# Optimization experiments

Hardware: AMD Instinct MI355X
Metric: run time of the kernel (lower is better)

## Reference

```python
import jax, jax.numpy as jnp
import numpy as np
from math import sqrt

THRESHOLD = 0.5
NEG_POS_RATIO = 3
ALPHA = 1.0


def make_priors():
    fms = [(38, 0.1, [1.0, 2.0, 0.5]), (19, 0.2, [1.0, 2.0, 0.5, 3.0, 1.0 / 3]),
           (10, 0.375, [1.0, 2.0, 0.5, 3.0, 1.0 / 3]), (5, 0.55, [1.0, 2.0, 0.5, 3.0, 1.0 / 3]),
           (3, 0.725, [1.0, 2.0, 0.5]), (1, 0.9, [1.0, 2.0, 0.5])]
    scales = [0.1, 0.2, 0.375, 0.55, 0.725, 0.9]
    priors = []
    for k, (d, s, ratios) in enumerate(fms):
        for i in range(d):
            for j in range(d):
                cx = (i + 0.5) / d
                cy = (j + 0.5) / d
                for r in ratios:
                    priors.append([cx, cy, s * sqrt(r), s / sqrt(r)])
                    if r == 1.0:
                        add = sqrt(scales[k] * scales[k + 1]) if k + 1 < len(scales) else 1.0
                        priors.append([cx, cy, add, add])
    return np.clip(np.asarray(priors, dtype=np.float32), 0.0, 1.0)  # [8732, 4]


def cxcy_to_xy(b):
    return jnp.concatenate([b[..., :2] - b[..., 2:] / 2.0, b[..., :2] + b[..., 2:] / 2.0], -1)


def jaccard(a, b):
    # a: [O,4] cxcy, b: [P,4] cxcy -> IoU [O,P]
    a_xy, b_xy = cxcy_to_xy(a), cxcy_to_xy(b)
    lt = jnp.maximum(a_xy[:, None, :2], b_xy[None, :, :2])
    rb = jnp.minimum(a_xy[:, None, 2:], b_xy[None, :, 2:])
    wh = jnp.clip(rb - lt, 0.0)
    inter = wh[..., 0] * wh[..., 1]
    area_a = (a_xy[:, 2] - a_xy[:, 0]) * (a_xy[:, 3] - a_xy[:, 1])
    area_b = (b_xy[:, 2] - b_xy[:, 0]) * (b_xy[:, 3] - b_xy[:, 1])
    return inter / (area_a[:, None] + area_b[None, :] - inter)


def cxcy_to_gcxgcy(cxcy, priors):
    g_cxcy = (cxcy[..., :2] - priors[..., :2]) / (priors[..., 2:] / 10.0)
    g_wh = jnp.log(cxcy[..., 2:] / priors[..., 2:]) * 5.0
    return jnp.concatenate([g_cxcy, g_wh], -1)


def match_one(boxes_i, priors):
    # boxes_i: [O,4] cxcy
    n_obj = boxes_i.shape[0]
    ov = jaccard(boxes_i, priors)                      # [O, P]
    ov_per_prior = ov.max(0)                           # [P]
    obj_per_prior = ov.argmax(0)                       # [P]
    prior_per_obj = ov.argmax(1)                       # [O]
    obj_per_prior = obj_per_prior.at[prior_per_obj].set(jnp.arange(n_obj))
    ov_per_prior = ov_per_prior.at[prior_per_obj].set(1.0)
    labels = (ov_per_prior >= THRESHOLD).astype(jnp.int32)  # [P], 1=text 0=bg
    true_locs = cxcy_to_gcxgcy(boxes_i[obj_per_prior], priors)  # [P,4]
    return labels, true_locs


def setup_inputs() -> dict:
    key = jax.random.key(0)
    k1, k2, k3, k4 = jax.random.split(key, 4)
    priors = jnp.asarray(make_priors())
    B, P, O = 512, priors.shape[0], 16
    predicted_locs = jax.random.normal(k1, (B, P, 4), dtype=jnp.float32)
    predicted_scores = jax.random.normal(k2, (B, P, 2), dtype=jnp.float32)
    centers = 0.2 + 0.6 * jax.random.uniform(k3, (B, O, 2), dtype=jnp.float32)
    wh = 0.05 + 0.35 * jax.random.uniform(k4, (B, O, 2), dtype=jnp.float32)
    boxes = jnp.concatenate([centers, wh], -1)  # cxcy format
    return {"predicted_locs": predicted_locs, "predicted_scores": predicted_scores,
            "boxes": boxes, "priors": priors}


def reference(predicted_locs, predicted_scores, boxes, priors):
    B, P, _ = predicted_locs.shape
    labels, true_locs = jax.vmap(match_one, in_axes=(0, None))(boxes, priors)  # [B,P], [B,P,4]
    pos = labels != 0
    mask = pos.astype(predicted_locs.dtype)            # [B,P]
    n_pos = pos.sum(1)                                 # [B]

    # localization L1 loss (mean over positive box coordinates)
    loc_abs = jnp.abs(predicted_locs - true_locs).sum(-1)  # [B,P]
    loc_loss = (loc_abs * mask).sum() / (mask.sum() * 4.0)

    # per-prior cross-entropy
    logp = jax.nn.log_softmax(predicted_scores, -1)
    ce = -jnp.take_along_axis(logp, labels[..., None], -1)[..., 0]  # [B,P]

    conf_pos = (ce * mask).sum()
    ce_neg = jnp.where(pos, 0.0, ce)
    ce_neg = jnp.sort(ce_neg, axis=1)[:, ::-1]         # descending
    hard = jnp.arange(P)[None, :] < (NEG_POS_RATIO * n_pos)[:, None]
    conf_hn = (ce_neg * hard.astype(ce_neg.dtype)).sum()
    conf_loss = (conf_pos + conf_hn) / n_pos.sum().astype(predicted_locs.dtype)
    return conf_loss + ALPHA * loc_loss
```

## Files before the change

kernel.cpp:

```cpp
#include <hip/hip_runtime.h>

#define NP 8732
#define NQ (NP / 4)
#define NPT 35
#define NO 16
#define BLK 256
#define NWAVE (BLK / 64)
#define SPLIT 4
#define CHUNK (NP / SPLIT)


__global__ __launch_bounds__(BLK, 8) void match_kernel(
    const float* __restrict__ boxes,
    const float* __restrict__ priors,
    unsigned char* __restrict__ g_obj,
    float* __restrict__ g_bv,
    int*   __restrict__ g_bi)
{
    const int b    = blockIdx.x;
    const int s    = blockIdx.y;
    const int tid  = threadIdx.x;
    const int lane = tid & 63;
    const int wv   = tid >> 6;
    const int quad = tid & 3;
    const int objLo = quad << 2;
    const int lo = s * CHUNK, hi = lo + CHUNK;

    __shared__ float s_bxy[NO][4];
    __shared__ float s_barea[NO];
    __shared__ float s_redv[NO * NWAVE];
    __shared__ int   s_redi[NO * NWAVE];

    if (tid < NO) {
        const float* bx = boxes + (size_t)b * NO * 4 + tid * 4;
        float cx = bx[0], cy = bx[1], w = bx[2], h = bx[3];
        s_bxy[tid][0] = cx - w * 0.5f; s_bxy[tid][1] = cy - h * 0.5f;
        s_bxy[tid][2] = cx + w * 0.5f; s_bxy[tid][3] = cy + h * 0.5f;
        s_barea[tid] = w * h;
    }
    __syncthreads();

    float rx0[4], ry0[4], rx1[4], ry1[4], ra[4];
#pragma unroll
    for (int j = 0; j < 4; j++) {
        rx0[j] = s_bxy[objLo + j][0]; ry0[j] = s_bxy[objLo + j][1];
        rx1[j] = s_bxy[objLo + j][2]; ry1[j] = s_bxy[objLo + j][3];
        ra[j]  = s_barea[objLo + j];
    }

    float tbv[4]; int tbp[4];
#pragma unroll
    for (int j = 0; j < 4; j++) { tbv[j] = -1.0f; tbp[j] = lo; }

    unsigned char* obj_row = g_obj + (size_t)b * NP;
    for (int p = lo + (tid >> 2); p < hi; p += (BLK / 4)) {
        float4 pr = ((const float4*)priors)[p];
        float px0 = pr.x - pr.z * 0.5f, py0 = pr.y - pr.w * 0.5f;
        float px1 = pr.x + pr.z * 0.5f, py1 = pr.y + pr.w * 0.5f;
        float areab = pr.z * pr.w;
        float bv = -1.0f; int bo = objLo;
#pragma unroll
        for (int j = 0; j < 4; j++) {
            float ix0 = fmaxf(rx0[j], px0);
            float iy0 = fmaxf(ry0[j], py0);
            float ix1 = fminf(rx1[j], px1);
            float iy1 = fminf(ry1[j], py1);
            float iw = fmaxf(ix1 - ix0, 0.0f);
            float ih = fmaxf(iy1 - iy0, 0.0f);
            float inter = iw * ih;
            float den = ra[j] + areab - inter;
            float iou = inter * __builtin_amdgcn_rcpf(den);
            if (iou > bv)     { bv = iou; bo = objLo + j; }
            if (iou > tbv[j]) { tbv[j] = iou; tbp[j] = p; }
        }
        float vN = __shfl_xor(bv, 1, 64);
        int   oN = __shfl_xor(bo, 1, 64);
        bool take = (quad & 1) ? (vN >= bv) : (vN > bv);
        if (take) { bv = vN; bo = oN; }
        vN = __shfl_xor(bv, 2, 64);
        oN = __shfl_xor(bo, 2, 64);
        take = (quad & 2) ? (vN >= bv) : (vN > bv);
        if (take) { bv = vN; bo = oN; }
        if (quad == 0) {
            bool pos = (bv >= 0.5f);
            obj_row[p] = (unsigned char)(bo | (pos ? 0x80 : 0));
        }
    }

#pragma unroll
    for (int j = 0; j < 4; j++) {
        float v = tbv[j]; int i = tbp[j];
        for (int off = 32; off >= 4; off >>= 1) {
            float v2 = __shfl_down(v, off, 64);
            int   i2 = __shfl_down(i, off, 64);
            if (v2 > v || (v2 == v && i2 < i)) { v = v2; i = i2; }
        }
        if (lane < 4) {
            s_redv[(objLo + j) * NWAVE + wv] = v;
            s_redi[(objLo + j) * NWAVE + wv] = i;
        }
    }
    __syncthreads();
    if (tid < NO) {
        float v = s_redv[tid * NWAVE]; int i = s_redi[tid * NWAVE];
#pragma unroll
        for (int w = 1; w < NWAVE; w++) {
            float v2 = s_redv[tid * NWAVE + w]; int i2 = s_redi[tid * NWAVE + w];
            if (v2 > v || (v2 == v && i2 < i)) { v = v2; i = i2; }
        }
        g_bv[((size_t)b * NO + tid) * SPLIT + s] = v;
        g_bi[((size_t)b * NO + tid) * SPLIT + s] = i;
    }
}

__device__ __forceinline__ int hist_select(unsigned* hist, unsigned* s_part,
                                           unsigned* s_csuf, unsigned* s_sel,
                                           unsigned& kk, int tid, int lane, int wv)
{
    unsigned ps = 0;
#pragma unroll
    for (int i = 0; i < 16; i++) ps += hist[tid * 16 + i];
    s_part[tid] = ps;
    __syncthreads();
    if (wv == 0) {
        unsigned c0 = s_part[4 * lane + 0], c1 = s_part[4 * lane + 1];
        unsigned c2 = s_part[4 * lane + 2], c3 = s_part[4 * lane + 3];
        unsigned g = c0 + c1 + c2 + c3;
        unsigned incl = g;
#pragma unroll
        for (int off = 1; off < 64; off <<= 1) {
            unsigned o = __shfl_down(incl, off, 64);
            if (lane + off < 64) incl += o;
        }
        unsigned excl = incl - g;
        s_csuf[4 * lane + 3] = excl;
        s_csuf[4 * lane + 2] = excl + c3;
        s_csuf[4 * lane + 1] = excl + c3 + c2;
        s_csuf[4 * lane + 0] = excl + c3 + c2 + c1;
    }
    __syncthreads();
    unsigned base = s_csuf[tid];
    if (base < kk && kk <= base + s_part[tid]) {
        unsigned run = base;
        for (int i = 15; i >= 0; i--) {
            unsigned h = hist[tid * 16 + i];
            if (kk <= run + h) { s_sel[0] = (unsigned)(tid * 16 + i); s_sel[1] = kk - run; break; }
            run += h;
        }
    }
    __syncthreads();
    kk = s_sel[1];
    return (int)s_sel[0];
}

__global__ __launch_bounds__(BLK, 2) void loss_kernel(
    const float* __restrict__ plocs,
    const float* __restrict__ pscores,
    const float* __restrict__ boxes,
    const float* __restrict__ priors,
    const unsigned char* __restrict__ g_obj,
    const float* __restrict__ g_bv,
    const int*   __restrict__ g_bi,
    float* __restrict__ loc_out,
    float* __restrict__ conf_out,
    int*   __restrict__ npos_out)
{
    const int b    = blockIdx.x;
    const int tid  = threadIdx.x;
    const int lane = tid & 63;
    const int wv   = tid >> 6;

    __shared__ unsigned char s_obj[NP];
    __shared__ unsigned s_hist[4096];
    __shared__ unsigned s_part[256];
    __shared__ unsigned s_csuf[256];
    __shared__ unsigned s_sel[2];
    __shared__ float s_bcw[NO][4];
    __shared__ int   s_bestp[NO];
    __shared__ float s_tval;
    __shared__ float s_fred[3 * NWAVE];
    __shared__ int   s_ired[NWAVE];

    const unsigned* objw = (const unsigned*)(g_obj + (size_t)b * NP);
    for (int i = tid; i < NP / 4; i += BLK) ((unsigned*)s_obj)[i] = objw[i];
    if (tid < NO * 4) ((float*)s_bcw)[tid] = boxes[(size_t)b * NO * 4 + tid];
    if (tid < NO) {
        const float* bv = g_bv + ((size_t)b * NO + tid) * SPLIT;
        const int*   bi = g_bi + ((size_t)b * NO + tid) * SPLIT;
        float v = bv[0]; int i = bi[0];
#pragma unroll
        for (int s = 1; s < SPLIT; s++) {
            float v2 = bv[s]; int i2 = bi[s];
            if (v2 > v || (v2 == v && i2 < i)) { v = v2; i = i2; }
        }
        s_bestp[tid] = i;
    }
    __syncthreads();
    if (tid == 0) {
#pragma unroll
        for (int o = 0; o < NO; o++) s_obj[s_bestp[o]] = (unsigned char)(0x80 | o);
    }
    __syncthreads();

    float ce[NPT];
    float loc_sum = 0.0f, conf_pos = 0.0f; int np = 0;
    const float2* sc2 = (const float2*)(pscores + (size_t)b * NP * 2);
    const float4* pl4 = (const float4*)(plocs  + (size_t)b * NP * 4);
#pragma unroll
    for (int k = 0; k < NPT; k++) {
        int p = tid + k * BLK;
        float v = 0.0f;
        if (p < NP) {
            unsigned m = s_obj[p];
            bool pos = (m & 0x80) != 0;
            float2 s = sc2[p];
            float mx = fmaxf(s.x, s.y);
            float dd = fabsf(s.x - s.y);
            float cev = mx + __logf(1.0f + __expf(-dd)) - (pos ? s.y : s.x);
            if (pos) {
                np++;
                conf_pos += cev;
                int o = m & 15;
                float4 pr = ((const float4*)priors)[p];
                float gx = (s_bcw[o][0] - pr.x) / (pr.z / 10.0f);
                float gy = (s_bcw[o][1] - pr.y) / (pr.w / 10.0f);
                float gw = __logf(s_bcw[o][2] / pr.z) * 5.0f;
                float gh = __logf(s_bcw[o][3] / pr.w) * 5.0f;
                float4 pl = pl4[p];
                loc_sum += fabsf(pl.x - gx) + fabsf(pl.y - gy)
                         + fabsf(pl.z - gw) + fabsf(pl.w - gh);
            } else {
                v = cev;
            }
        }
        ce[k] = v;
    }

    int npw = np;
    for (int off = 32; off; off >>= 1) npw += __shfl_down(npw, off, 64);
    if (lane == 0) s_ired[wv] = npw;
    __syncthreads();
    int n_pos = 0;
#pragma unroll
    for (int w = 0; w < NWAVE; w++) n_pos += s_ired[w];

    const int K = 3 * n_pos;
    const bool selAll = (K >= NP);
    float t = 0.0f;
    if (!selAll) {
        unsigned kk = (unsigned)K;
        for (int i = tid; i < 4096; i += BLK) s_hist[i] = 0u;
        __syncthreads();
#pragma unroll
        for (int k = 0; k < NPT; k++)
            atomicAdd(&s_hist[__float_as_uint(ce[k]) >> 19], 1u);
        __syncthreads();
        unsigned b1 = (unsigned)hist_select(s_hist, s_part, s_csuf, s_sel, kk, tid, lane, wv);
        unsigned cnt1 = s_hist[b1];
        if (cnt1 == 1u) {
#pragma unroll
            for (int k = 0; k < NPT; k++)
                if ((__float_as_uint(ce[k]) >> 19) == b1) s_tval = ce[k];
            __syncthreads();
            t = s_tval;
        } else {
            __syncthreads();
            for (int i = tid; i < 4096; i += BLK) s_hist[i] = 0u;
            __syncthreads();
#pragma unroll
            for (int k = 0; k < NPT; k++) {
                unsigned u = __float_as_uint(ce[k]);
                if ((u >> 19) == b1) atomicAdd(&s_hist[(u >> 7) & 0xFFFu], 1u);
            }
            __syncthreads();
            unsigned b2 = (unsigned)hist_select(s_hist, s_part, s_csuf, s_sel, kk, tid, lane, wv);
            unsigned p2 = (b1 << 12) | b2;
            unsigned cnt2 = s_hist[b2];
            if (cnt2 == 1u) {
#pragma unroll
                for (int k = 0; k < NPT; k++)
                    if ((__float_as_uint(ce[k]) >> 7) == p2) s_tval = ce[k];
                __syncthreads();
                t = s_tval;
            } else {
                __syncthreads();
                for (int i = tid; i < 4096; i += BLK) s_hist[i] = 0u;
                __syncthreads();
#pragma unroll
                for (int k = 0; k < NPT; k++) {
                    unsigned u = __float_as_uint(ce[k]);
                    if ((u >> 7) == p2) atomicAdd(&s_hist[u & 0x7Fu], 1u);
                }
                __syncthreads();
                unsigned b3 = (unsigned)hist_select(s_hist, s_part, s_csuf, s_sel, kk, tid, lane, wv);
                t = __uint_as_float((p2 << 7) | b3);
            }
        }
    }

    float sgt = 0.0f; int cgt = 0;
#pragma unroll
    for (int k = 0; k < NPT; k++) {
        float v = ce[k];
        if (selAll || v > t) { sgt += v; cgt++; }
    }

    float a = sgt, c = conf_pos, l = loc_sum; int g = cgt;
    for (int off = 32; off; off >>= 1) {
        a += __shfl_down(a, off, 64);
        c += __shfl_down(c, off, 64);
        l += __shfl_down(l, off, 64);
        g += __shfl_down(g, off, 64);
    }
    __syncthreads();
    if (lane == 0) {
        s_fred[wv] = a; s_fred[NWAVE + wv] = c; s_fred[2 * NWAVE + wv] = l;
        s_ired[wv] = g;
    }
    __syncthreads();
    if (tid == 0) {
        float sa = 0.0f, sc = 0.0f, sl = 0.0f; int sg = 0;
#pragma unroll
        for (int w = 0; w < NWAVE; w++) {
            sa += s_fred[w]; sc += s_fred[NWAVE + w]; sl += s_fred[2 * NWAVE + w];
            sg += s_ired[w];
        }
        float conf_hn = selAll ? sa : (sa + (float)(K - sg) * t);
        conf_out[b] = sc + conf_hn;
        loc_out[b]  = sl;
        npos_out[b] = n_pos;
    }
}

__global__ __launch_bounds__(BLK, 2) void mbox_row_kernel(
    const float* __restrict__ plocs, const float* __restrict__ pscores,
    const float* __restrict__ boxes, const float* __restrict__ priors,
    float* __restrict__ loc_out, float* __restrict__ conf_out,
    int* __restrict__ npos_out)
{
    const int b = blockIdx.x, tid = threadIdx.x, lane = tid & 63, wv = tid >> 6;
    const int par = tid & 1, objLo = par << 3;
    __shared__ __align__(16) float s_ce[NP];
    __shared__ unsigned char s_obj[NP];
    __shared__ float s_bcw[NO][4], s_bxy[NO][4], s_barea[NO];
    __shared__ float s_redv[NO * NWAVE]; __shared__ int s_redi[NO * NWAVE];
    __shared__ int s_bestp[NO];
    __shared__ unsigned s_hist16[16];
    __shared__ float s_tval;
    __shared__ float s_fred[3 * NWAVE]; __shared__ int s_ired[NWAVE];

    if (tid < NO * 4) ((float*)s_bcw)[tid] = boxes[(size_t)b * NO * 4 + tid];
    __syncthreads();
    if (tid < NO) {
        float cx = s_bcw[tid][0], cy = s_bcw[tid][1], w = s_bcw[tid][2], h = s_bcw[tid][3];
        s_bxy[tid][0] = cx - w * 0.5f; s_bxy[tid][1] = cy - h * 0.5f;
        s_bxy[tid][2] = cx + w * 0.5f; s_bxy[tid][3] = cy + h * 0.5f;
        s_barea[tid] = w * h;
    }
    __syncthreads();
    float rx0[8], ry0[8], rx1[8], ry1[8], ra[8];
#pragma unroll
    for (int j = 0; j < 8; j++) {
        rx0[j] = s_bxy[objLo + j][0]; ry0[j] = s_bxy[objLo + j][1];
        rx1[j] = s_bxy[objLo + j][2]; ry1[j] = s_bxy[objLo + j][3];
        ra[j]  = s_barea[objLo + j];
    }
    float tbv[8]; int tbp[8];
#pragma unroll
    for (int j = 0; j < 8; j++) { tbv[j] = -1.0f; tbp[j] = 0; }
    for (int p = (tid >> 1); p < NP; p += (BLK / 2)) {
        float4 pr = ((const float4*)priors)[p];
        float px0 = pr.x - pr.z * 0.5f, py0 = pr.y - pr.w * 0.5f;
        float px1 = pr.x + pr.z * 0.5f, py1 = pr.y + pr.w * 0.5f;
        float areab = pr.z * pr.w;
        float bv = -1.0f; int bo = objLo;
#pragma unroll
        for (int j = 0; j < 8; j++) {
            float ix0 = fmaxf(rx0[j], px0), iy0 = fmaxf(ry0[j], py0);
            float ix1 = fminf(rx1[j], px1), iy1 = fminf(ry1[j], py1);
            float iw = fmaxf(ix1 - ix0, 0.0f), ih = fmaxf(iy1 - iy0, 0.0f);
            float inter = iw * ih, den = ra[j] + areab - inter;
            float iou = inter * __builtin_amdgcn_rcpf(den);
            if (iou > bv) { bv = iou; bo = objLo + j; }
            if (iou > tbv[j]) { tbv[j] = iou; tbp[j] = p; }
        }
        float vN = __shfl_xor(bv, 1, 64); int oN = __shfl_xor(bo, 1, 64);
        bool take = par ? (vN >= bv) : (vN > bv);
        if (take) { bv = vN; bo = oN; }
        if (par == 0) s_obj[p] = (unsigned char)(bo | ((bv >= 0.5f) ? 0x80 : 0));
    }
#pragma unroll
    for (int j = 0; j < 8; j++) {
        float v = tbv[j]; int i = tbp[j];
        for (int off = 32; off >= 2; off >>= 1) {
            float v2 = __shfl_down(v, off, 64); int i2 = __shfl_down(i, off, 64);
            if (v2 > v || (v2 == v && i2 < i)) { v = v2; i = i2; }
        }
        if (lane < 2) { s_redv[(objLo + j) * NWAVE + wv] = v; s_redi[(objLo + j) * NWAVE + wv] = i; }
    }
    __syncthreads();
    if (tid < NO) {
        float v = s_redv[tid * NWAVE]; int i = s_redi[tid * NWAVE];
#pragma unroll
        for (int w = 1; w < NWAVE; w++) {
            float v2 = s_redv[tid * NWAVE + w]; int i2 = s_redi[tid * NWAVE + w];
            if (v2 > v || (v2 == v && i2 < i)) { v = v2; i = i2; }
        }
        s_bestp[tid] = i;
    }
    __syncthreads();
    if (tid == 0) {
#pragma unroll
        for (int o = 0; o < NO; o++) s_obj[s_bestp[o]] = (unsigned char)(0x80 | o);
    }
    __syncthreads();
    float loc_sum = 0.0f, conf_pos = 0.0f; int np = 0;
    const float2* sc2 = (const float2*)(pscores + (size_t)b * NP * 2);
    const float4* pl4 = (const float4*)(plocs + (size_t)b * NP * 4);
    for (int p = tid; p < NP; p += BLK) {
        unsigned m = s_obj[p]; bool pos = (m & 0x80) != 0;
        float2 s = sc2[p];
        float mx = fmaxf(s.x, s.y), dd = fabsf(s.x - s.y);
        float cev = mx + __logf(1.0f + __expf(-dd)) - (pos ? s.y : s.x);
        if (pos) {
            np++; conf_pos += cev;
            int o = m & 15;
            float4 pr = ((const float4*)priors)[p];
            float gx = (s_bcw[o][0] - pr.x) / (pr.z / 10.0f);
            float gy = (s_bcw[o][1] - pr.y) / (pr.w / 10.0f);
            float gw = __logf(s_bcw[o][2] / pr.z) * 5.0f;
            float gh = __logf(s_bcw[o][3] / pr.w) * 5.0f;
            float4 pl = pl4[p];
            loc_sum += fabsf(pl.x - gx) + fabsf(pl.y - gy) + fabsf(pl.z - gw) + fabsf(pl.w - gh);
            s_ce[p] = 0.0f;
        } else s_ce[p] = cev;
    }
    int npw = np;
    for (int off = 32; off; off >>= 1) npw += __shfl_down(npw, off, 64);
    if (lane == 0) s_ired[wv] = npw;
    __syncthreads();
    int n_pos = 0;
#pragma unroll
    for (int w = 0; w < NWAVE; w++) n_pos += s_ired[w];
    const int K = 3 * n_pos; const bool selAll = (K >= NP);
    float t = 0.0f;
    const float4* ce4 = (const float4*)s_ce;
    if (!selAll) {
        unsigned prefix = 0u, kk = (unsigned)K; bool done = false;
        for (int shift = 28; shift >= 0 && !done; shift -= 4) {
            __syncthreads();
            if (tid < 16) s_hist16[tid] = 0u;
            __syncthreads();
            unsigned maskhi = (shift == 28) ? 0u : (0xFFFFFFFFu << (shift + 4));
            for (int q = tid; q < NQ; q += BLK) {
                float4 v = ce4[q];
#pragma unroll
                for (int j = 0; j < 4; j++) {
                    unsigned u = __float_as_uint(j == 0 ? v.x : j == 1 ? v.y : j == 2 ? v.z : v.w);
                    if ((u & maskhi) == prefix) atomicAdd(&s_hist16[(u >> shift) & 15u], 1u);
                }
            }
            __syncthreads();
            int dsel = 15; unsigned cnt;
            for (;; dsel--) { cnt = s_hist16[dsel]; if (kk <= cnt || dsel == 0) break; kk -= cnt; }
            prefix |= ((unsigned)dsel << shift);
            if (shift > 0 && cnt == 1u) {
                unsigned mh = 0xFFFFFFFFu << shift;
                for (int q = tid; q < NQ; q += BLK) {
                    float4 v = ce4[q];
#pragma unroll
                    for (int j = 0; j < 4; j++) {
                        float f = (j == 0 ? v.x : j == 1 ? v.y : j == 2 ? v.z : v.w);
                        if ((__float_as_uint(f) & mh) == prefix) s_tval = f;
                    }
                }
                __syncthreads();
                t = s_tval; done = true;
            } else if (shift == 0) t = __uint_as_float(prefix);
        }
    }
    float sgt = 0.0f; int cgt = 0;
    for (int q = tid; q < NQ; q += BLK) {
        float4 v = ce4[q];
        if (selAll || v.x > t) { sgt += v.x; cgt++; }
        if (selAll || v.y > t) { sgt += v.y; cgt++; }
        if (selAll || v.z > t) { sgt += v.z; cgt++; }
        if (selAll || v.w > t) { sgt += v.w; cgt++; }
    }
    float a = sgt, c = conf_pos, l = loc_sum; int g = cgt;
    for (int off = 32; off; off >>= 1) {
        a += __shfl_down(a, off, 64); c += __shfl_down(c, off, 64);
        l += __shfl_down(l, off, 64); g += __shfl_down(g, off, 64);
    }
    __syncthreads();
    if (lane == 0) { s_fred[wv] = a; s_fred[NWAVE + wv] = c; s_fred[2 * NWAVE + wv] = l; s_ired[wv] = g; }
    __syncthreads();
    if (tid == 0) {
        float sa = 0, sc = 0, sl = 0; int sg = 0;
#pragma unroll
        for (int w = 0; w < NWAVE; w++) { sa += s_fred[w]; sc += s_fred[NWAVE + w]; sl += s_fred[2 * NWAVE + w]; sg += s_ired[w]; }
        float conf_hn = selAll ? sa : (sa + (float)(K - sg) * t);
        conf_out[b] = sc + conf_hn; loc_out[b] = sl; npos_out[b] = n_pos;
    }
}

__global__ __launch_bounds__(256) void mbox_finalize_kernel(
    const float* __restrict__ loc_in, const float* __restrict__ conf_in,
    const int* __restrict__ npos_in, int B, float* __restrict__ out)
{
    __shared__ float sl[4], sc[4];
    __shared__ int si[4];
    int tid = threadIdx.x, lane = tid & 63, wv = tid >> 6;
    float l = 0.0f, c = 0.0f; int n = 0;
    for (int i = tid; i < B; i += 256) { l += loc_in[i]; c += conf_in[i]; n += npos_in[i]; }
    for (int off = 32; off; off >>= 1) {
        l += __shfl_down(l, off, 64);
        c += __shfl_down(c, off, 64);
        n += __shfl_down(n, off, 64);
    }
    if (lane == 0) { sl[wv] = l; sc[wv] = c; si[wv] = n; }
    __syncthreads();
    if (tid == 0) {
        float tl = sl[0] + sl[1] + sl[2] + sl[3];
        float tc = sc[0] + sc[1] + sc[2] + sc[3];
        int tn = si[0] + si[1] + si[2] + si[3];
        float fn = (float)tn;
        out[0] = tc / fn + tl / (fn * 4.0f);
    }
}

extern "C" void kernel_launch(void* const* d_in, const int* in_sizes, int n_in,
                              void* d_out, int out_size, void* d_ws, size_t ws_size,
                              hipStream_t stream) {
    const float* plocs   = (const float*)d_in[0];
    const float* pscores = (const float*)d_in[1];
    const float* boxes   = (const float*)d_in[2];
    const float* priors  = (const float*)d_in[3];
    const int B = in_sizes[0] / (NP * 4);

    float* loc_ws  = (float*)d_ws;
    float* conf_ws = loc_ws + B;
    int*   np_ws   = (int*)(conf_ws + B);
    float* g_bv    = (float*)(np_ws + B);
    int*   g_bi    = (int*)(g_bv + (size_t)B * NO * SPLIT);
    unsigned char* g_obj = (unsigned char*)(g_bi + (size_t)B * NO * SPLIT);
    size_t need = (size_t)(3 * B) * 4 + (size_t)B * NO * SPLIT * 8 + (size_t)B * NP;

    if (ws_size >= need) {
        match_kernel<<<dim3(B, SPLIT), BLK, 0, stream>>>(boxes, priors, g_obj, g_bv, g_bi);
        loss_kernel<<<B, BLK, 0, stream>>>(plocs, pscores, boxes, priors,
                                           g_obj, g_bv, g_bi, loc_ws, conf_ws, np_ws);
    } else {
        mbox_row_kernel<<<B, BLK, 0, stream>>>(plocs, pscores, boxes, priors,
                                               loc_ws, conf_ws, np_ws);
    }
    mbox_finalize_kernel<<<1, 256, 0, stream>>>(loc_ws, conf_ws, np_ws, B, (float*)d_out);
}
```

Baseline: 197.9 us.

## Process one prior per thread over all objects with overlap-skip in matching

The match kernel now assigns one prior per thread and loops over all 16 objects, replacing the quad-per-prior scheme and its cross-lane shuffles. Box coordinates are loaded straight from global memory into wave-uniform scalar registers via readfirstlane instead of through shared memory. The IoU math is skipped when the box and prior do not overlap. The per-object argmax reduction is restructured to match the new layout, and launch bounds drop to 4 blocks per CU to allow more registers. This trades higher register pressure and branch divergence for less redundant work and no shuffles in the hot loop.

```diff
diff --git a/kernel.cpp b/kernel.cpp
--- a/kernel.cpp
+++ b/kernel.cpp
@@ -8,9 +8,14 @@
 #define NWAVE (BLK / 64)
 #define SPLIT 4
 #define CHUNK (NP / SPLIT)
-
-
-__global__ __launch_bounds__(BLK, 8) void match_kernel(
+#define NITER ((CHUNK + BLK - 1) / BLK)
+
+
+__device__ __forceinline__ float rfl(float x) {
+    return __uint_as_float(__builtin_amdgcn_readfirstlane(__float_as_uint(x)));
+}
+
+__global__ __launch_bounds__(BLK, 4) void match_kernel(
     const float* __restrict__ boxes,
     const float* __restrict__ priors,
     unsigned char* __restrict__ g_obj,
@@ -22,94 +27,87 @@
     const int tid  = threadIdx.x;
     const int lane = tid & 63;
     const int wv   = tid >> 6;
-    const int quad = tid & 3;
-    const int objLo = quad << 2;
     const int lo = s * CHUNK, hi = lo + CHUNK;
 
-    __shared__ float s_bxy[NO][4];
-    __shared__ float s_barea[NO];
-    __shared__ float s_redv[NO * NWAVE];
-    __shared__ int   s_redi[NO * NWAVE];
-
-    if (tid < NO) {
-        const float* bx = boxes + (size_t)b * NO * 4 + tid * 4;
-        float cx = bx[0], cy = bx[1], w = bx[2], h = bx[3];
-        s_bxy[tid][0] = cx - w * 0.5f; s_bxy[tid][1] = cy - h * 0.5f;
-        s_bxy[tid][2] = cx + w * 0.5f; s_bxy[tid][3] = cy + h * 0.5f;
-        s_barea[tid] = w * h;
-    }
-    __syncthreads();
-
-    float rx0[4], ry0[4], rx1[4], ry1[4], ra[4];
-#pragma unroll
-    for (int j = 0; j < 4; j++) {
-        rx0[j] = s_bxy[objLo + j][0]; ry0[j] = s_bxy[objLo + j][1];
-        rx1[j] = s_bxy[objLo + j][2]; ry1[j] = s_bxy[objLo + j][3];
-        ra[j]  = s_barea[objLo + j];
-    }
-
-    float tbv[4]; int tbp[4];
-#pragma unroll
-    for (int j = 0; j < 4; j++) { tbv[j] = -1.0f; tbp[j] = lo; }
+    __shared__ float s_pv[NWAVE][NO][16];
+    __shared__ int   s_pi[NWAVE][NO][16];
+
+    float sx0[NO], sy0[NO], sx1[NO], sy1[NO], ra[NO];
+    {
+        const float4* bx4 = (const float4*)(boxes + (size_t)b * NO * 4);
+#pragma unroll
+        for (int j = 0; j < NO; j++) {
+            float4 o = bx4[j];
+            float hx = o.z * 0.5f, hy = o.w * 0.5f;
+            sx0[j] = rfl(o.x - hx); sy0[j] = rfl(o.y - hy);
+            sx1[j] = rfl(o.x + hx); sy1[j] = rfl(o.y + hy);
+            ra[j]  = o.z * o.w;
+        }
+    }
+
+    float tbv[NO]; int tbp[NO];
+#pragma unroll
+    for (int j = 0; j < NO; j++) { tbv[j] = -1.0f; tbp[j] = lo; }
 
     unsigned char* obj_row = g_obj + (size_t)b * NP;
-    for (int p = lo + (tid >> 2); p < hi; p += (BLK / 4)) {
+    for (int k = 0; k < NITER; k++) {
+        int p0 = lo + tid + k * BLK;
+        bool valid = p0 < hi;
+        int p = valid ? p0 : hi - 1;
         float4 pr = ((const float4*)priors)[p];
         float px0 = pr.x - pr.z * 0.5f, py0 = pr.y - pr.w * 0.5f;
         float px1 = pr.x + pr.z * 0.5f, py1 = pr.y + pr.w * 0.5f;
         float areab = pr.z * pr.w;
-        float bv = -1.0f; int bo = objLo;
-#pragma unroll
-        for (int j = 0; j < 4; j++) {
-            float ix0 = fmaxf(rx0[j], px0);
-            float iy0 = fmaxf(ry0[j], py0);
-            float ix1 = fminf(rx1[j], px1);
-            float iy1 = fminf(ry1[j], py1);
-            float iw = fmaxf(ix1 - ix0, 0.0f);
-            float ih = fmaxf(iy1 - iy0, 0.0f);
-            float inter = iw * ih;
-            float den = ra[j] + areab - inter;
-            float iou = inter * __builtin_amdgcn_rcpf(den);
-            if (iou > bv)     { bv = iou; bo = objLo + j; }
-            if (iou > tbv[j]) { tbv[j] = iou; tbp[j] = p; }
-        }
-        float vN = __shfl_xor(bv, 1, 64);
-        int   oN = __shfl_xor(bo, 1, 64);
-        bool take = (quad & 1) ? (vN >= bv) : (vN > bv);
-        if (take) { bv = vN; bo = oN; }
-        vN = __shfl_xor(bv, 2, 64);
-        oN = __shfl_xor(bo, 2, 64);
-        take = (quad & 2) ? (vN >= bv) : (vN > bv);
-        if (take) { bv = vN; bo = oN; }
-        if (quad == 0) {
-            bool pos = (bv >= 0.5f);
-            obj_row[p] = (unsigned char)(bo | (pos ? 0x80 : 0));
-        }
-    }
-
-#pragma unroll
-    for (int j = 0; j < 4; j++) {
+        if (!valid) px0 = 4.0f;
+        float bv = -1.0f; int bo = 0;
+#pragma unroll
+        for (int j = 0; j < NO; j++) {
+            bool ov = (sx1[j] >= px0) && (px1 >= sx0[j]) &&
+                      (sy1[j] >= py0) && (py1 >= sy0[j]);
+            if (ov) {
+                float ix0 = fmaxf(sx0[j], px0);
+                float iy0 = fmaxf(sy0[j], py0);
+                float ix1 = fminf(sx1[j], px1);
+                float iy1 = fminf(sy1[j], py1);
+                float iw = fmaxf(ix1 - ix0, 0.0f);
+                float ih = fmaxf(iy1 - iy0, 0.0f);
+                float inter = iw * ih;
+                float den = ra[j] + areab - inter;
+                float iou = inter * __builtin_amdgcn_rcpf(den);
+                if (iou > bv)     { bv = iou; bo = j; }
+                if (iou > tbv[j]) { tbv[j] = iou; tbp[j] = p; }
+            }
+        }
+        if (valid) obj_row[p] = (unsigned char)(bo | ((bv >= 0.5f) ? 0x80 : 0));
+    }
+
+#pragma unroll
+    for (int j = 0; j < NO; j++) {
         float v = tbv[j]; int i = tbp[j];
-        for (int off = 32; off >= 4; off >>= 1) {
-            float v2 = __shfl_down(v, off, 64);
-            int   i2 = __shfl_down(i, off, 64);
+        float v2 = __shfl_down(v, 32, 64); int i2 = __shfl_down(i, 32, 64);
+        if (v2 > v || (v2 == v && i2 < i)) { v = v2; i = i2; }
+        v2 = __shfl_down(v, 16, 64); i2 = __shfl_down(i, 16, 64);
+        if (v2 > v || (v2 == v && i2 < i)) { v = v2; i = i2; }
+        if (lane < 16) { s_pv[wv][j][lane] = v; s_pi[wv][j][lane] = i; }
+    }
+    __syncthreads();
+    {
+        const int j = tid >> 4, e = tid & 15;
+        float v = s_pv[0][j][e]; int i = s_pi[0][j][e];
+#pragma unroll
+        for (int w = 1; w < NWAVE; w++) {
+            float v2 = s_pv[w][j][e]; int i2 = s_pi[w][j][e];
             if (v2 > v || (v2 == v && i2 < i)) { v = v2; i = i2; }
         }
-        if (lane < 4) {
-            s_redv[(objLo + j) * NWAVE + wv] = v;
-            s_redi[(objLo + j) * NWAVE + wv] = i;
-        }
-    }
-    __syncthreads();
-    if (tid < NO) {
-        float v = s_redv[tid * NWAVE]; int i = s_redi[tid * NWAVE];
-#pragma unroll
-        for (int w = 1; w < NWAVE; w++) {
-            float v2 = s_redv[tid * NWAVE + w]; int i2 = s_redi[tid * NWAVE + w];
+#pragma unroll
+        for (int off = 8; off >= 1; off >>= 1) {
+            float v2 = __shfl_down(v, off, 16); int i2 = __shfl_down(i, off, 16);
             if (v2 > v || (v2 == v && i2 < i)) { v = v2; i = i2; }
         }
-        g_bv[((size_t)b * NO + tid) * SPLIT + s] = v;
-        g_bi[((size_t)b * NO + tid) * SPLIT + s] = i;
+        if (e == 0) {
+            g_bv[((size_t)b * NO + j) * SPLIT + s] = v;
+            g_bi[((size_t)b * NO + j) * SPLIT + s] = i;
+        }
     }
 }
 
```

Result: no change. 194.6 us (-1.7%).
